# Optimization experiments

Hardware: AMD Instinct MI355X
Metric: run time of the kernel (lower is better)

The kernel has to match this reference:

```python
import jax, jax.numpy as jnp
import numpy as np

NUM_HEADS = 16
HEAD_SIZE = 64
HIDDEN = NUM_HEADS * HEAD_SIZE  # 1024


def setup_inputs() -> dict:
    key = jax.random.key(0)
    ks = jax.random.split(key, 9)
    B, S1, S2 = 8, 1024, 1024
    scale = 1.0 / np.sqrt(HIDDEN)
    inp = {
        "s1_hidden_states": jax.random.normal(ks[0], (B, S1, HIDDEN), jnp.float32),
        "s2_hidden_states": jax.random.normal(ks[1], (B, S2, HIDDEN), jnp.float32),
        "s2_attention_mask": jnp.zeros((B, 1, 1, S2), jnp.float32),
        "Wq": jax.random.normal(ks[2], (HIDDEN, HIDDEN), jnp.float32) * scale,
        "bq": jnp.zeros((HIDDEN,), jnp.float32),
        "Wk": jax.random.normal(ks[3], (HIDDEN, HIDDEN), jnp.float32) * scale,
        "bk": jnp.zeros((HIDDEN,), jnp.float32),
        "Wv": jax.random.normal(ks[4], (HIDDEN, HIDDEN), jnp.float32) * scale,
        "bv": jnp.zeros((HIDDEN,), jnp.float32),
        "cl_att": 1,
    }
    return inp


def _split_heads(x):
    # [B, S, H*D] -> [B, H, S, D]
    B, S, _ = x.shape
    return x.reshape(B, S, NUM_HEADS, HEAD_SIZE).transpose(0, 2, 1, 3)


def reference(s1_hidden_states, s2_hidden_states, s2_attention_mask,
              Wq, bq, Wk, bk, Wv, bv, cl_att):
    q = _split_heads(s1_hidden_states @ Wq + bq)  # [B,H,S1,D]
    k = _split_heads(s2_hidden_states @ Wk + bk)  # [B,H,S2,D]
    v = _split_heads(s2_hidden_states @ Wv + bv)  # [B,H,S2,D]

    scores = jnp.einsum("bhqd,bhkd->bhqk", q, k) / np.sqrt(HEAD_SIZE)
    scores = scores + s2_attention_mask  # broadcast [B,1,1,S2]
    probs = jax.nn.softmax(scores, axis=-1)
    if cl_att:
        probs = jax.nn.softmax(1.0 - probs + s2_attention_mask, axis=-1)
    # dropout is identity in eval/reference mode
    ctx = jnp.einsum("bhqk,bhkd->bhqd", probs, v)  # [B,H,S1,D]
    B, _, S1, _ = ctx.shape
    return ctx.transpose(0, 2, 1, 3).reshape(B, S1, HIDDEN)
```

## Files before the change

### kernel.cpp

```cpp
#include <hip/hip_runtime.h>
#include <hip/hip_bf16.h>

typedef unsigned short u16;
typedef __attribute__((ext_vector_type(8))) short bf16x8;
typedef __attribute__((ext_vector_type(4))) float f32x4;
typedef __attribute__((ext_vector_type(4))) unsigned u32x4;

#define L2E 1.4426950408889634f

__device__ __forceinline__ u16 f2bf(float f) {
  unsigned u = __float_as_uint(f);
  u = u + 0x7fffu + ((u >> 16) & 1u);
  return (u16)(u >> 16);
}
__device__ __forceinline__ unsigned cvtpk(float a, float b) {
  unsigned r;
  asm("v_cvt_pk_bf16_f32 %0, %1, %2" : "=v"(r) : "v"(a), "v"(b));
  return r;
}
__device__ __forceinline__ float lo16(unsigned v) { return __uint_as_float(v << 16); }
__device__ __forceinline__ float hi16(unsigned v) { return __uint_as_float(v & 0xffff0000u); }

__global__ void conv2_f32_bf16(const float* __restrict__ a, const float* __restrict__ b,
                               u16* __restrict__ o, int n4a, int n4tot) {
  int i = blockIdx.x * blockDim.x + threadIdx.x;
  int stride = gridDim.x * blockDim.x;
  for (; i < n4tot; i += stride) {
    float4 v = (i < n4a) ? ((const float4*)a)[i] : ((const float4*)b)[i - n4a];
    ushort4 ov = make_ushort4(f2bf(v.x), f2bf(v.y), f2bf(v.z), f2bf(v.w));
    ((ushort4*)o)[i] = ov;
  }
}

__global__ void wtrans3(const float* __restrict__ Wq, const float* __restrict__ Wk,
                        const float* __restrict__ Wv,
                        u16* __restrict__ Wtq, u16* __restrict__ Wtk, u16* __restrict__ Wtv) {
  int z = blockIdx.z;
  const float* W = (z == 0) ? Wq : (z == 1) ? Wk : Wv;
  u16* Wt = (z == 0) ? Wtq : (z == 1) ? Wtk : Wtv;
  __shared__ float T[32][33];
  int k0 = blockIdx.y * 32, n0 = blockIdx.x * 32;
  int tx = threadIdx.x, ty = threadIdx.y;
  #pragma unroll
  for (int j = 0; j < 4; ++j) T[ty + 8*j][tx] = W[(size_t)(k0 + ty + 8*j) * 1024 + n0 + tx];
  __syncthreads();
  #pragma unroll
  for (int j = 0; j < 4; ++j) Wt[(size_t)(n0 + ty + 8*j) * 1024 + k0 + tx] = f2bf(T[tx][ty + 8*j]);
}

__global__ __launch_bounds__(256) void qkv_gemm3(const u16* __restrict__ X1, const u16* __restrict__ X2,
                                                 const u16* __restrict__ Wtq, const u16* __restrict__ Wtk,
                                                 const u16* __restrict__ Wtv,
                                                 const float* __restrict__ bq, const float* __restrict__ bk,
                                                 const float* __restrict__ bv,
                                                 u16* __restrict__ Qo, u16* __restrict__ Ko, u16* __restrict__ Vo) {
  int bid = blockIdx.x;
  int xcd = bid & 7, idx = bid >> 3;
  int nblk = idx & 7, pair = idx >> 3;
  int zy = xcd * 24 + pair;
  int z = zy >> 6, y = zy & 63;
  int m0 = y * 128, n0 = nblk * 128;

  const u16* X   = (z == 0) ? X1 : X2;
  const u16* Wt  = (z == 0) ? Wtq : (z == 1) ? Wtk : Wtv;
  const float* bias = (z == 0) ? bq : (z == 1) ? bk : bv;
  u16* outp = (z == 0) ? Qo : (z == 1) ? Ko : Vo;

  __shared__ __align__(16) u16 As[2][128 * 32];
  __shared__ __align__(16) u16 Bs[2][128 * 32];
  int tid = threadIdx.x;
  int w = tid >> 6, l = tid & 63;
  int wm = w >> 1, wn = w & 1;
  int lq = l & 15, g = l >> 4;
  const int4* Xs = (const int4*)X;
  const int4* Ws = (const int4*)Wt;

#define QSTAGE(bi, kt) do { _Pragma("unroll")                                                \
    for (int c_ = 0; c_ < 2; ++c_) {                                                        \
      int i_ = c_ * 256 + tid;                                      \
      int row_ = i_ >> 2, kc_ = (i_ & 3) ^ ((row_ >> 1) & 3);                               \
      __builtin_amdgcn_global_load_lds(                                                     \
          (const __attribute__((address_space(1))) void*)&Xs[(size_t)(m0 + row_) * 128 + (kt) * 4 + kc_], \
          (__attribute__((address_space(3))) void*)&((int4*)As[bi])[i_], 16, 0, 0);         \
      __builtin_amdgcn_global_load_lds(                                                     \
          (const __attribute__((address_space(1))) void*)&Ws[(size_t)(n0 + row_) * 128 + (kt) * 4 + kc_], \
          (__attribute__((address_space(3))) void*)&((int4*)Bs[bi])[i_], 16, 0, 0);         \
    } } while (0)

  int aOff[4], bOff[4];
  #pragma unroll
  for (int mc = 0; mc < 4; ++mc) {
    int rowA = wm * 64 + mc * 16 + lq;
    aOff[mc] = rowA * 32 + ((g ^ ((rowA >> 1) & 3)) * 8);
    int rowB = wn * 64 + mc * 16 + lq;
    bOff[mc] = rowB * 32 + ((g ^ ((rowB >> 1) & 3)) * 8);
  }

  f32x4 acc[4][4] = {};
  QSTAGE(0, 0);
  __syncthreads();
  int cur = 0;
  for (int kt = 0; kt < 32; ++kt) {
    if (kt < 31) QSTAGE(cur ^ 1, kt + 1);
    bf16x8 a[4], bb[4];
    #pragma unroll
    for (int mc = 0; mc < 4; ++mc) a[mc]  = *(const bf16x8*)&As[cur][aOff[mc]];
    #pragma unroll
    for (int nc = 0; nc < 4; ++nc) bb[nc] = *(const bf16x8*)&Bs[cur][bOff[nc]];
    #pragma unroll
    for (int mc = 0; mc < 4; ++mc)
      #pragma unroll
      for (int nc = 0; nc < 4; ++nc)
        acc[mc][nc] = __builtin_amdgcn_mfma_f32_16x16x32_bf16(a[mc], bb[nc], acc[mc][nc], 0, 0, 0);
    __syncthreads();
    cur ^= 1;
  }
#undef QSTAGE
  #pragma unroll
  for (int nc = 0; nc < 4; ++nc) {
    int n = n0 + wn * 64 + nc * 16 + lq;
    float bvv = bias[n];
    int h = n >> 6, d = n & 63;
    #pragma unroll
    for (int mc = 0; mc < 4; ++mc) {
      int srow_base = m0 + wm * 64 + mc * 16 + g * 4;
      if (z == 2) {
        int b = srow_base >> 10, s = srow_base & 1023;
        ushort4 vv;
        vv.x = f2bf(acc[mc][nc][0] + bvv);
        vv.y = f2bf(acc[mc][nc][1] + bvv);
        vv.z = f2bf(acc[mc][nc][2] + bvv);
        vv.w = f2bf(acc[mc][nc][3] + bvv);
        *(ushort4*)&outp[((size_t)((b * 16 + h) * 64 + d)) * 1024 + s] = vv;
      } else {
        #pragma unroll
        for (int r = 0; r < 4; ++r) {
          int sm = srow_base + r;
          int b = sm >> 10, s = sm & 1023;
          outp[((size_t)((b * 16 + h) * 1024 + s)) * 64 + d] = f2bf(acc[mc][nc][r] + bvv);
        }
      }
    }
  }
}

__global__ __launch_bounds__(256, 2) void attn16(const u16* __restrict__ Q, const u16* __restrict__ K,
                                                 const u16* __restrict__ Vt, const float* __restrict__ mask,
                                                 const int* __restrict__ clp, float* __restrict__ out) {
  __shared__ __align__(16) u16 KVl[2][8192];
  __shared__ __align__(16) float maskL2[1024];
  __shared__ float z1p[4][32];
  __shared__ float z2p[4][32];

  int bid = blockIdx.x;
  int xcd = bid & 7, idx = bid >> 3;
  int bh = xcd * 16 + (idx >> 5);
  int qt = idx & 31;
  int b = bh >> 4, h = bh & 15;
  int tid = threadIdx.x;
  int w = tid >> 6, l = tid & 63;
  int lq = l & 15, g = l >> 4;
  int qb = qt * 32;

  const u16* Kb = K + (size_t)bh * 65536;
  const u16* Vb = Vt + (size_t)bh * 65536;
  int cl = clp[0];

  const u16* kS[4]; int kD[4];
  #pragma unroll
  for (int c_ = 0; c_ < 4; ++c_) {
    int i_ = c_ * 256 + tid, row_ = i_ >> 3, ch_ = i_ & 7;
    int f_ = (row_ & 3) | ((((row_ >> 3) ^ (row_ >> 4)) & 1) << 2);
    kS[c_] = Kb + row_ * 64 + (ch_ ^ f_) * 8;
    kD[c_] = i_ * 8;
  }
  const u16* vS[4]; int vD[4];
  #pragma unroll
  for (int c_ = 0; c_ < 4; ++c_) {
    int i_ = c_ * 256 + tid, row_ = i_ >> 4, ch_ = i_ & 15;
    vS[c_] = Vb + row_ * 1024 + (ch_ ^ (row_ & 15)) * 8;
    vD[c_] = i_ * 8;
  }

#define STAGE_K(bi, t) do { _Pragma("unroll")                                                 \
    for (int c_ = 0; c_ < 4; ++c_)                                                           \
      __builtin_amdgcn_global_load_lds(                                                      \
        (const __attribute__((address_space(1))) void*)(kS[c_] + (t) * 8192),                \
        (__attribute__((address_space(3))) void*)&KVl[bi][kD[c_]], 16, 0, 0); } while (0)

#define STAGE_V(bi, t) do { _Pragma("unroll")                                                 \
    for (int c_ = 0; c_ < 4; ++c_)                                                           \
      __builtin_amdgcn_global_load_lds(                                                      \
        (const __attribute__((address_space(1))) void*)(vS[c_] + (t) * 128),                 \
        (__attribute__((address_space(3))) void*)&KVl[bi][vD[c_]], 16, 0, 0); } while (0)

  STAGE_K(0, 0);

  for (int i = tid; i < 1024; i += 256) maskL2[i] = mask[b * 1024 + i] * L2E;

  bf16x8 qf[2][2];
  #pragma unroll
  for (int qg = 0; qg < 2; ++qg) {
    const u16* Qp = Q + ((size_t)bh * 1024 + qb + qg * 16 + lq) * 64 + g * 8;
    qf[qg][0] = *(const bf16x8*)Qp;
    qf[qg][1] = *(const bf16x8*)(Qp + 32);
  }

  int kOff[2][2];
  #pragma unroll
  for (int c = 0; c < 2; ++c) {
    int row128 = w * 32 + ((lq >> 2) << 3) + c * 4 + (lq & 3);
    int F = (row128 & 3) | ((((row128 >> 3) ^ (row128 >> 4)) & 1) << 2);
    kOff[c][0] = row128 * 64 + ((g ^ F) * 8);
    kOff[c][1] = row128 * 64 + (((g + 4) ^ F) * 8);
  }
  int vOff[4];
  #pragma unroll
  for (int dc = 0; dc < 4; ++dc) {
    int row = dc * 16 + lq;
    vOff[dc] = row * 128 + (((w * 4 + g) ^ (row & 15)) * 8);
  }
  int mBase = w * 32 + g * 8;

  __syncthreads();

  const float sl2e = 0.125f * L2E;
  unsigned sp[64];
  float z1[2] = {0.f, 0.f};
  int cur = 0;
  #pragma unroll
  for (int t = 0; t < 8; ++t) {
    if (t < 7) STAGE_K(cur ^ 1, t + 1);
    else       STAGE_V(0, 0);
    #pragma unroll
    for (int c = 0; c < 2; ++c) {
      bf16x8 kf0 = *(const bf16x8*)&KVl[cur][kOff[c][0]];
      bf16x8 kf1 = *(const bf16x8*)&KVl[cur][kOff[c][1]];
      const float4 mk = *(const float4*)&maskL2[t * 128 + mBase + c * 4];
      #pragma unroll
      for (int qg = 0; qg < 2; ++qg) {
        f32x4 tt = {0.f, 0.f, 0.f, 0.f};
        tt = __builtin_amdgcn_mfma_f32_16x16x32_bf16(kf0, qf[qg][0], tt, 0, 0, 0);
        tt = __builtin_amdgcn_mfma_f32_16x16x32_bf16(kf1, qf[qg][1], tt, 0, 0, 0);
        float e0 = __builtin_amdgcn_exp2f(fmaf(tt[0], sl2e, mk.x));
        float e1 = __builtin_amdgcn_exp2f(fmaf(tt[1], sl2e, mk.y));
        float e2 = __builtin_amdgcn_exp2f(fmaf(tt[2], sl2e, mk.z));
        float e3 = __builtin_amdgcn_exp2f(fmaf(tt[3], sl2e, mk.w));
        z1[qg] += (e0 + e1) + (e2 + e3);
        sp[t * 8 + qg * 4 + c * 2 + 0] = cvtpk(e0, e1);
        sp[t * 8 + qg * 4 + c * 2 + 1] = cvtpk(e2, e3);
      }
    }
    __syncthreads();
    cur ^= 1;
  }

  #pragma unroll
  for (int qg = 0; qg < 2; ++qg) {
    z1[qg] += __shfl_xor(z1[qg], 16);
    z1[qg] += __shfl_xor(z1[qg], 32);
  }
  if (l < 16) { z1p[w][l] = z1[0]; z1p[w][16 + l] = z1[1]; }
  __syncthreads();
  float cr[2];
  #pragma unroll
  for (int qg = 0; qg < 2; ++qg) {
    int q = qg * 16 + lq;
    float Z1 = (z1p[0][q] + z1p[1][q]) + (z1p[2][q] + z1p[3][q]);
    cr[qg] = L2E * __builtin_amdgcn_rcpf(Z1);
  }

  f32x4 acc[2][4] = {};
  float z2[2] = {0.f, 0.f};
  #pragma unroll
  for (int t = 0; t < 8; ++t) {
    if (t < 7) STAGE_V((t + 1) & 1, t + 1);
    u32x4 pk[2];
    #pragma unroll
    for (int qg = 0; qg < 2; ++qg) {
      if (cl) {
        #pragma unroll
        for (int j = 0; j < 4; ++j) {
          unsigned e = sp[t * 8 + qg * 4 + j];
          float mkA = maskL2[t * 128 + mBase + 2 * j];
          float mkB = maskL2[t * 128 + mBase + 2 * j + 1];
          float pA = __builtin_amdgcn_exp2f(fmaf(-cr[qg], lo16(e), mkA));
          float pB = __builtin_amdgcn_exp2f(fmaf(-cr[qg], hi16(e), mkB));
          z2[qg] += pA + pB;
          pk[qg][j] = cvtpk(pA, pB);
        }
      } else {
        pk[qg] = *(u32x4*)&sp[t * 8 + qg * 4];
      }
    }
    #pragma unroll
    for (int dc = 0; dc < 4; ++dc) {
      bf16x8 vf = *(const bf16x8*)&KVl[t & 1][vOff[dc]];
      #pragma unroll
      for (int qg = 0; qg < 2; ++qg)
        acc[qg][dc] = __builtin_amdgcn_mfma_f32_16x16x32_bf16(
            __builtin_bit_cast(bf16x8, pk[qg]), vf, acc[qg][dc], 0, 0, 0);
    }
    if (t < 7) __syncthreads();
  }

  #pragma unroll
  for (int qg = 0; qg < 2; ++qg) {
    z2[qg] += __shfl_xor(z2[qg], 16);
    z2[qg] += __shfl_xor(z2[qg], 32);
  }
  if (l < 16) { z2p[w][l] = z2[0]; z2p[w][16 + l] = z2[1]; }
  __syncthreads();
  float* redF = (float*)&KVl[0][0];
  if (w > 0) {
    #pragma unroll
    for (int qg = 0; qg < 2; ++qg)
      #pragma unroll
      for (int dc = 0; dc < 4; ++dc)
        #pragma unroll
        for (int r = 0; r < 4; ++r)
          redF[(w - 1) * 2176 + (qg * 16 + g * 4 + r) * 68 + dc * 16 + lq] = acc[qg][dc][r];
  }
  __syncthreads();
  if (w == 0) {
    #pragma unroll
    for (int qg = 0; qg < 2; ++qg) {
      #pragma unroll
      for (int r = 0; r < 4; ++r) {
        int q = qg * 16 + g * 4 + r;
        float phi;
        if (cl) {
          float Z2 = (z2p[0][q] + z2p[1][q]) + (z2p[2][q] + z2p[3][q]);
          phi = __builtin_amdgcn_rcpf(Z2);
        } else {
          float Z1 = (z1p[0][q] + z1p[1][q]) + (z1p[2][q] + z1p[3][q]);
          phi = __builtin_amdgcn_rcpf(Z1);
        }
        size_t orow = ((size_t)(b * 1024 + qb + q)) * 1024 + h * 64;
        #pragma unroll
        for (int dc = 0; dc < 4; ++dc) {
          int dq = q * 68 + dc * 16 + lq;
          float o = acc[qg][dc][r] + redF[dq] + redF[2176 + dq] + redF[4352 + dq];
          out[orow + dc * 16 + lq] = o * phi;
        }
      }
    }
  }
#undef STAGE_K
#undef STAGE_V
}

extern "C" void kernel_launch(void* const* d_in, const int* in_sizes, int n_in,
                              void* d_out, int out_size, void* d_ws, size_t ws_size,
                              hipStream_t stream) {
  const float* s1   = (const float*)d_in[0];
  const float* s2   = (const float*)d_in[1];
  const float* mask = (const float*)d_in[2];
  const float* Wq   = (const float*)d_in[3];
  const float* bq   = (const float*)d_in[4];
  const float* Wk   = (const float*)d_in[5];
  const float* bk   = (const float*)d_in[6];
  const float* Wv   = (const float*)d_in[7];
  const float* bv   = (const float*)d_in[8];
  const int*   cl   = (const int*)d_in[9];
  float* out = (float*)d_out;

  u16* ws  = (u16*)d_ws;
  const size_t M1 = 1024 * 1024;
  u16* X1  = ws;
  u16* Wtq = ws + 16 * M1;
  u16* Wtk = Wtq + M1;
  u16* Wtv = Wtk + M1;
  u16* Qb  = Wtv + M1;
  u16* Kb  = Qb + 8 * M1;
  u16* Vtb = Kb + 8 * M1;
  u16* X2  = ws + 8 * M1;

  conv2_f32_bf16<<<2048, 256, 0, stream>>>(s1, s2, X1, 2097152, 4194304);
  wtrans3<<<dim3(32, 32, 3), dim3(32, 8), 0, stream>>>(Wq, Wk, Wv, Wtq, Wtk, Wtv);
  qkv_gemm3<<<1536, 256, 0, stream>>>(X1, X2, Wtq, Wtk, Wtv, bq, bk, bv, Qb, Kb, Vtb);
  attn16<<<4096, 256, 0, stream>>>(Qb, Kb, Vtb, mask, cl, out);
}
```

Before: 176.9 us.

## Fuse fp32-to-bf16 activation conversion into QKV GEMM A-tile loads

Drops the separate conversion kernel that wrote bf16 copies of both hidden-state tensors. The GEMM now reads fp32 activations straight from global memory into registers and packs them to bf16 with v_cvt_pk_bf16_f32. It writes them into the swizzled LDS A tile after the MFMA work of the current step, so the loads overlap compute. This removes a launch and a full read/write pass over the activations, at the cost of doubled A-operand global traffic per GEMM (fp32, reread by each of the 8 N-blocks) and extra register use.

```diff
diff --git a/kernel.cpp b/kernel.cpp
--- a/kernel.cpp
+++ b/kernel.cpp
@@ -20,17 +20,6 @@
 }
 __device__ __forceinline__ float lo16(unsigned v) { return __uint_as_float(v << 16); }
 __device__ __forceinline__ float hi16(unsigned v) { return __uint_as_float(v & 0xffff0000u); }
-
-__global__ void conv2_f32_bf16(const float* __restrict__ a, const float* __restrict__ b,
-                               u16* __restrict__ o, int n4a, int n4tot) {
-  int i = blockIdx.x * blockDim.x + threadIdx.x;
-  int stride = gridDim.x * blockDim.x;
-  for (; i < n4tot; i += stride) {
-    float4 v = (i < n4a) ? ((const float4*)a)[i] : ((const float4*)b)[i - n4a];
-    ushort4 ov = make_ushort4(f2bf(v.x), f2bf(v.y), f2bf(v.z), f2bf(v.w));
-    ((ushort4*)o)[i] = ov;
-  }
-}
 
 __global__ void wtrans3(const float* __restrict__ Wq, const float* __restrict__ Wk,
                         const float* __restrict__ Wv,
@@ -48,7 +37,7 @@
   for (int j = 0; j < 4; ++j) Wt[(size_t)(n0 + ty + 8*j) * 1024 + k0 + tx] = f2bf(T[tx][ty + 8*j]);
 }
 
-__global__ __launch_bounds__(256) void qkv_gemm3(const u16* __restrict__ X1, const u16* __restrict__ X2,
+__global__ __launch_bounds__(256) void qkv_gemm3(const float* __restrict__ S1, const float* __restrict__ S2,
                                                  const u16* __restrict__ Wtq, const u16* __restrict__ Wtk,
                                                  const u16* __restrict__ Wtv,
                                                  const float* __restrict__ bq, const float* __restrict__ bk,
@@ -61,7 +50,7 @@
   int z = zy >> 6, y = zy & 63;
   int m0 = y * 128, n0 = nblk * 128;
 
-  const u16* X   = (z == 0) ? X1 : X2;
+  const float* Xf  = (z == 0) ? S1 : S2;
   const u16* Wt  = (z == 0) ? Wtq : (z == 1) ? Wtk : Wtv;
   const float* bias = (z == 0) ? bq : (z == 1) ? bk : bv;
   u16* outp = (z == 0) ? Qo : (z == 1) ? Ko : Vo;
@@ -72,19 +61,40 @@
   int w = tid >> 6, l = tid & 63;
   int wm = w >> 1, wn = w & 1;
   int lq = l & 15, g = l >> 4;
-  const int4* Xs = (const int4*)X;
   const int4* Ws = (const int4*)Wt;
 
-#define QSTAGE(bi, kt) do { _Pragma("unroll")                                                \
+  const float4* aSrc[2]; int aDst[2];
+  #pragma unroll
+  for (int c_ = 0; c_ < 2; ++c_) {
+    int i_ = c_ * 256 + tid;
+    int row_ = i_ >> 2, kc_ = (i_ & 3) ^ ((row_ >> 1) & 3);
+    aSrc[c_] = (const float4*)(Xf + (size_t)(m0 + row_) * 1024 + kc_ * 8);
+    aDst[c_] = i_;
+  }
+
+#define BSTAGE(bi, kt) do { _Pragma("unroll")                                                \
     for (int c_ = 0; c_ < 2; ++c_) {                                                        \
-      int i_ = c_ * 256 + tid;                                      \
+      int i_ = c_ * 256 + tid;                                                              \
       int row_ = i_ >> 2, kc_ = (i_ & 3) ^ ((row_ >> 1) & 3);                               \
-      __builtin_amdgcn_global_load_lds(                                                     \
-          (const __attribute__((address_space(1))) void*)&Xs[(size_t)(m0 + row_) * 128 + (kt) * 4 + kc_], \
-          (__attribute__((address_space(3))) void*)&((int4*)As[bi])[i_], 16, 0, 0);         \
       __builtin_amdgcn_global_load_lds(                                                     \
           (const __attribute__((address_space(1))) void*)&Ws[(size_t)(n0 + row_) * 128 + (kt) * 4 + kc_], \
           (__attribute__((address_space(3))) void*)&((int4*)Bs[bi])[i_], 16, 0, 0);         \
+    } } while (0)
+
+#define ALOAD(kt) do { _Pragma("unroll")                                                    \
+    for (int c_ = 0; c_ < 2; ++c_) {                                                        \
+      xa[c_][0] = aSrc[c_][(kt) * 8];                                                       \
+      xa[c_][1] = aSrc[c_][(kt) * 8 + 1];                                                   \
+    } } while (0)
+
+#define AWRITE(bi) do { _Pragma("unroll")                                                   \
+    for (int c_ = 0; c_ < 2; ++c_) {                                                        \
+      u32x4 pk_;                                                                            \
+      pk_[0] = cvtpk(xa[c_][0].x, xa[c_][0].y);                                             \
+      pk_[1] = cvtpk(xa[c_][0].z, xa[c_][0].w);                                             \
+      pk_[2] = cvtpk(xa[c_][1].x, xa[c_][1].y);                                             \
+      pk_[3] = cvtpk(xa[c_][1].z, xa[c_][1].w);                                             \
+      *(u32x4*)&As[bi][aDst[c_] * 8] = pk_;                                                 \
     } } while (0)
 
   int aOff[4], bOff[4];
@@ -97,11 +107,17 @@
   }
 
   f32x4 acc[4][4] = {};
-  QSTAGE(0, 0);
+  float4 xa[2][2];
+  ALOAD(0);
+  BSTAGE(0, 0);
+  AWRITE(0);
   __syncthreads();
   int cur = 0;
   for (int kt = 0; kt < 32; ++kt) {
-    if (kt < 31) QSTAGE(cur ^ 1, kt + 1);
+    if (kt < 31) {
+      ALOAD(kt + 1);
+      BSTAGE(cur ^ 1, kt + 1);
+    }
     bf16x8 a[4], bb[4];
     #pragma unroll
     for (int mc = 0; mc < 4; ++mc) a[mc]  = *(const bf16x8*)&As[cur][aOff[mc]];
@@ -112,10 +128,13 @@
       #pragma unroll
       for (int nc = 0; nc < 4; ++nc)
         acc[mc][nc] = __builtin_amdgcn_mfma_f32_16x16x32_bf16(a[mc], bb[nc], acc[mc][nc], 0, 0, 0);
+    if (kt < 31) AWRITE(cur ^ 1);
     __syncthreads();
     cur ^= 1;
   }
-#undef QSTAGE
+#undef BSTAGE
+#undef ALOAD
+#undef AWRITE
   #pragma unroll
   for (int nc = 0; nc < 4; ++nc) {
     int n = n0 + wn * 64 + nc * 16 + lq;
@@ -367,17 +386,14 @@
 
   u16* ws  = (u16*)d_ws;
   const size_t M1 = 1024 * 1024;
-  u16* X1  = ws;
   u16* Wtq = ws + 16 * M1;
   u16* Wtk = Wtq + M1;
   u16* Wtv = Wtk + M1;
   u16* Qb  = Wtv + M1;
   u16* Kb  = Qb + 8 * M1;
   u16* Vtb = Kb + 8 * M1;
-  u16* X2  = ws + 8 * M1;
-
-  conv2_f32_bf16<<<2048, 256, 0, stream>>>(s1, s2, X1, 2097152, 4194304);
+
   wtrans3<<<dim3(32, 32, 3), dim3(32, 8), 0, stream>>>(Wq, Wk, Wv, Wtq, Wtk, Wtv);
-  qkv_gemm3<<<1536, 256, 0, stream>>>(X1, X2, Wtq, Wtk, Wtv, bq, bk, bv, Qb, Kb, Vtb);
+  qkv_gemm3<<<1536, 256, 0, stream>>>(s1, s2, Wtq, Wtk, Wtv, bq, bk, bv, Qb, Kb, Vtb);
   attn16<<<4096, 256, 0, stream>>>(Qb, Kb, Vtb, mask, cl, out);
 }
```

New measurement: 173.7 us. Within noise of the previous version (-1.8%).
